# Kernel tuning notes

Measured on AMD Instinct MI355X. Metric: run time of the kernel, lower is better.

## Reference

```python
import jax, jax.numpy as jnp
import numpy as np

B, T, C, H = 2, 2048, 1024, 16
D = C // H
THETA = 10000.0


def setup_inputs() -> dict:
    key = jax.random.key(0)
    k1, k2, k3 = jax.random.split(key, 3)
    x = jax.random.normal(k1, (B, T, C), dtype=jnp.float32)
    tok_mask = jnp.ones((B, T), dtype=bool)
    # torch Linear weights stored transposed: y = x @ W.T; we store [in, out]
    W_qkv = jax.random.normal(k2, (C, 3 * C), dtype=jnp.float32) / np.sqrt(C)
    W_o = jax.random.normal(k3, (C, C), dtype=jnp.float32) / np.sqrt(C)
    return {"x": x, "tok_mask": tok_mask, "W_qkv": W_qkv, "W_o": W_o}


def _rope_tables(t_len):
    # NOTE: source uses exponents arange(1, D+1, 2)/D and positions starting at 1
    exps = jnp.arange(1, D + 1, 2, dtype=jnp.float32)[: D // 2] / D
    w = 1.0 / (THETA ** exps)                      # [D/2]
    t = jnp.arange(1, t_len + 1, dtype=jnp.float32)  # [T]
    ang = t[:, None] * w[None, :]                  # [T, D/2]
    return jnp.sin(ang), jnp.cos(ang)


def _rope(x, sin, cos):
    # x: [B, H, T, D]; rotate interleaved pairs
    x1 = x[..., ::2]
    x2 = x[..., 1::2]
    r1 = x1 * cos - x2 * sin
    r2 = x1 * sin + x2 * cos
    return jnp.stack((r1, r2), axis=-1).reshape(x.shape)


def reference(x, tok_mask, W_qkv, W_o):
    b, t, c = x.shape
    qkv = x @ W_qkv                                   # [B,T,3C]
    q, k, v = jnp.split(qkv, 3, axis=-1)
    def heads(z):
        return z.reshape(b, t, H, D).transpose(0, 2, 1, 3)  # [B,H,T,D]
    q, k, v = heads(q), heads(k), heads(v)
    sin, cos = _rope_tables(t)
    q = _rope(q, sin, cos)
    k = _rope(k, sin, cos)
    scores = jnp.einsum('bhqd,bhkd->bhqk', q, k) / jnp.sqrt(jnp.float32(D))
    # mask[b,i,j] = tok_mask[b,i] & tok_mask[b,j] & causal
    mask = tok_mask[:, None, :, None] & tok_mask[:, None, None, :]  # [B,1,T,T]
    causal = jnp.tril(jnp.ones((t, t), dtype=bool))
    mask = mask & causal[None, None, :, :]
    scores = jnp.where(mask, scores, jnp.float32(-1e9))
    att = jax.nn.softmax(scores, axis=-1)             # dropout p=0 (eval)
    y = jnp.einsum('bhqk,bhkd->bhqd', att, v)
    y = y.transpose(0, 2, 1, 3).reshape(b, t, c)
    return y @ W_o
```

## Files before the change

kernel.cpp:

```cpp
#include <hip/hip_runtime.h>
#include <hip/hip_bf16.h>

typedef __bf16 bf16x8 __attribute__((ext_vector_type(8)));
typedef short s16x4 __attribute__((ext_vector_type(4)));
typedef float floatx4 __attribute__((ext_vector_type(4)));
typedef __hip_bfloat16 bf16;

#define T_SEQ 2048
#define NH 16
#define HD 64
#define CDIM 1024

__device__ __forceinline__ void gload16(const bf16* g, bf16* ldsbase) {
  __builtin_amdgcn_global_load_lds((const __attribute__((address_space(1))) void*)g,
                                   (__attribute__((address_space(3))) void*)ldsbase, 16, 0, 0);
}

__global__ __launch_bounds__(256) void prep_kernel(const float* __restrict__ x,
                                                   const float* __restrict__ Wqkv,
                                                   const float* __restrict__ Wo,
                                                   bf16* __restrict__ Xb,
                                                   bf16* __restrict__ WqkvT,
                                                   bf16* __restrict__ WoT,
                                                   float2* __restrict__ tab) {
  __shared__ float tile[32][33];
  const int bid = blockIdx.x, tid = threadIdx.x;
  if (bid < 4096) {
    int i = bid * 256 + tid;
    const float4 v = ((const float4*)x)[i];
    union { bf16 h[4]; uint2 u; } pk;
    pk.h[0] = __float2bfloat16(v.x);
    pk.h[1] = __float2bfloat16(v.y);
    pk.h[2] = __float2bfloat16(v.z);
    pk.h[3] = __float2bfloat16(v.w);
    ((uint2*)Xb)[i] = pk.u;
  } else if (bid < 8192) {
    const float* in;
    bf16* out;
    int bx, by, R, Cc;
    if (bid < 7168) {
      int t = bid - 4096;
      in = Wqkv; out = WqkvT; R = 1024; Cc = 3072;
      bx = (t % 96) * 32; by = (t / 96) * 32;
    } else {
      int t = bid - 7168;
      in = Wo; out = WoT; R = 1024; Cc = 1024;
      bx = (t & 31) * 32; by = (t >> 5) * 32;
    }
    const int tx = tid & 31, ty = tid >> 5;
#pragma unroll
    for (int i = 0; i < 32; i += 8)
      tile[ty + i][tx] = in[(size_t)(by + ty + i) * Cc + bx + tx];
    __syncthreads();
#pragma unroll
    for (int i = 0; i < 32; i += 8)
      out[(size_t)(bx + ty + i) * R + by + tx] = __float2bfloat16(tile[tx][ty + i]);
  } else {
    int idx = (bid - 8192) * 256 + tid;
    int t = idx >> 5, j = idx & 31;
    float w = exp2f(-13.287712379549449f * (float)(2 * j + 1) * (1.0f / 64.0f));
    float ang = (float)(t + 1) * w;
    tab[idx] = make_float2(cosf(ang), sinf(ang));
  }
}

template <int MODE>
__global__ __launch_bounds__(256) void gemm_bt(
    const bf16* __restrict__ A, const bf16* __restrict__ BT, float* __restrict__ CoutF,
    const float2* __restrict__ tab, bf16* __restrict__ Qr, bf16* __restrict__ Kr,
    bf16* __restrict__ Vt, int M, int N, int K) {
  constexpr int LDK = 64;
  __shared__ __align__(16) bf16 As[128 * LDK];
  __shared__ __align__(16) bf16 Bs[128 * LDK];
  const int tid = threadIdx.x, lane = tid & 63, wave = tid >> 6;
  const int quad = lane >> 4, c16 = lane & 15;
  const int tile_m = blockIdx.y * 128, tile_n = blockIdx.x * 128;
  const int wm = (wave >> 1) * 64, wn = (wave & 1) * 64;
  const int r0 = tid >> 3;
  const int csw = ((tid & 7) ^ (r0 & 7)) * 8;
  const int s1 = (quad ^ (c16 & 7)) * 8;
  const int s2 = s1 ^ 32;
  floatx4 acc[4][4] = {};
  for (int k0 = 0; k0 < K; k0 += 64) {
    __syncthreads();
#pragma unroll
    for (int i = 0; i < 4; i++) {
      gload16(&A[(size_t)(tile_m + r0 + i * 32) * K + k0 + csw], &As[i * 2048 + wave * 512]);
      gload16(&BT[(size_t)(tile_n + r0 + i * 32) * K + k0 + csw], &Bs[i * 2048 + wave * 512]);
    }
    __syncthreads();
    bf16x8 af[4], bfr[4];
#pragma unroll
    for (int i = 0; i < 4; i++) {
      af[i] = *(const bf16x8*)&As[(wm + i * 16 + c16) * LDK + s1];
      bfr[i] = *(const bf16x8*)&Bs[(wn + i * 16 + c16) * LDK + s1];
    }
#pragma unroll
    for (int mi = 0; mi < 4; mi++)
#pragma unroll
      for (int ni = 0; ni < 4; ni++)
        acc[mi][ni] = __builtin_amdgcn_mfma_f32_16x16x32_bf16(af[mi], bfr[ni], acc[mi][ni], 0, 0, 0);
#pragma unroll
    for (int i = 0; i < 4; i++) {
      af[i] = *(const bf16x8*)&As[(wm + i * 16 + c16) * LDK + s2];
      bfr[i] = *(const bf16x8*)&Bs[(wn + i * 16 + c16) * LDK + s2];
    }
#pragma unroll
    for (int mi = 0; mi < 4; mi++)
#pragma unroll
      for (int ni = 0; ni < 4; ni++)
        acc[mi][ni] = __builtin_amdgcn_mfma_f32_16x16x32_bf16(af[mi], bfr[ni], acc[mi][ni], 0, 0, 0);
  }
  if (MODE == 0) {
#pragma unroll
    for (int mi = 0; mi < 4; mi++) {
      int row0 = tile_m + wm + mi * 16 + quad * 4;
#pragma unroll
      for (int ni = 0; ni < 4; ni++) {
        int col = tile_n + wn + ni * 16 + c16;
#pragma unroll
        for (int r = 0; r < 4; r++)
          CoutF[(size_t)(row0 + r) * N + col] = acc[mi][ni][r];
      }
    }
  } else {
#pragma unroll
    for (int ni = 0; ni < 4; ni++) {
      int colg = tile_n + wn + ni * 16 + c16;
      int seg = colg >> 10;
      int cc = colg & 1023;
      int h = cc >> 6, d = cc & 63, j = d >> 1;
#pragma unroll
      for (int mi = 0; mi < 4; mi++) {
        int row0 = tile_m + wm + mi * 16 + quad * 4;
#pragma unroll
        for (int r = 0; r < 4; r++) {
          int rowg = row0 + r;
          int b = rowg >> 11, t = rowg & 2047;
          float val = acc[mi][ni][r];
          float partner = __shfl_xor(val, 1, 64);
          size_t bh = (size_t)(b * NH + h);
          if (seg == 2) {
            Vt[(bh * HD + d) * T_SEQ + t] = __float2bfloat16(val);
          } else {
            float2 sc = tab[t * 32 + j];
            float outv = ((d & 1) == 0) ? (val * sc.x - partner * sc.y)
                                        : (val * sc.x + partner * sc.y);
            if (seg == 0) outv *= 0.125f;
            bf16* dst = (seg == 0) ? Qr : Kr;
            dst[(bh * T_SEQ + t) * HD + d] = __float2bfloat16(outv);
          }
        }
      }
    }
  }
}

__global__ __launch_bounds__(256) void attn_kernel(const bf16* __restrict__ Qr,
                                                   const bf16* __restrict__ Kr,
                                                   const bf16* __restrict__ Vt,
                                                   bf16* __restrict__ Y) {
  constexpr int DPAD = 68;
  constexpr float FM = 5.0f;
  __shared__ __align__(16) bf16 Ks0[64 * DPAD], Ks1[64 * DPAD];
  __shared__ __align__(16) bf16 Vs0[64 * DPAD], Vs1[64 * DPAD];
  __shared__ __align__(16) bf16 Ps0[4][16 * DPAD], Ps1[4][16 * DPAD];
  const int qtile = 31 - (blockIdx.x >> 5), bh = blockIdx.x & 31;
  const int b = bh >> 4, h = bh & 15;
  const int tid = threadIdx.x, lane = tid & 63, wave = tid >> 6;
  const int quad = lane >> 4, c16 = lane & 15;
  const size_t hoff = (size_t)bh * T_SEQ * HD;
  const int row0 = tid >> 3, cp = tid & 7;
  const int qbase = qtile * 64;
  const int qg = qbase + wave * 16 + c16;
  bf16x8 qf0 = *(const bf16x8*)&Qr[hoff + (size_t)qg * HD + quad * 8];
  bf16x8 qf1 = *(const bf16x8*)&Qr[hoff + (size_t)qg * HD + 32 + quad * 8];
  floatx4 o_acc[4] = {};
  float l_run = 0.f;
  const int n_st = (qtile + 2) >> 1;
  bf16x8 kreg0 = *(const bf16x8*)&Kr[hoff + (size_t)row0 * HD + cp * 8];
  bf16x8 kreg1 = *(const bf16x8*)&Kr[hoff + (size_t)(row0 + 32) * HD + cp * 8];
  bf16x8 kreg2 = *(const bf16x8*)&Kr[hoff + (size_t)(row0 + 64) * HD + cp * 8];
  bf16x8 kreg3 = *(const bf16x8*)&Kr[hoff + (size_t)(row0 + 96) * HD + cp * 8];
  bf16x8 vreg0 = *(const bf16x8*)&Vt[hoff + (size_t)row0 * T_SEQ + cp * 8];
  bf16x8 vreg1 = *(const bf16x8*)&Vt[hoff + (size_t)(row0 + 32) * T_SEQ + cp * 8];
  bf16x8 vreg2 = *(const bf16x8*)&Vt[hoff + (size_t)row0 * T_SEQ + 64 + cp * 8];
  bf16x8 vreg3 = *(const bf16x8*)&Vt[hoff + (size_t)(row0 + 32) * T_SEQ + 64 + cp * 8];
  for (int st = 0; st < n_st; ++st) {
    const int sbase = st * 128;
    *(bf16x8*)&Ks0[row0 * DPAD + cp * 8] = kreg0;
    *(bf16x8*)&Ks0[(row0 + 32) * DPAD + cp * 8] = kreg1;
    *(bf16x8*)&Ks1[row0 * DPAD + cp * 8] = kreg2;
    *(bf16x8*)&Ks1[(row0 + 32) * DPAD + cp * 8] = kreg3;
    *(bf16x8*)&Vs0[row0 * DPAD + cp * 8] = vreg0;
    *(bf16x8*)&Vs0[(row0 + 32) * DPAD + cp * 8] = vreg1;
    *(bf16x8*)&Vs1[row0 * DPAD + cp * 8] = vreg2;
    *(bf16x8*)&Vs1[(row0 + 32) * DPAD + cp * 8] = vreg3;
    __syncthreads();
    if (st + 1 < n_st) {
      const int nb = sbase + 128;
      kreg0 = *(const bf16x8*)&Kr[hoff + (size_t)(nb + row0) * HD + cp * 8];
      kreg1 = *(const bf16x8*)&Kr[hoff + (size_t)(nb + row0 + 32) * HD + cp * 8];
      kreg2 = *(const bf16x8*)&Kr[hoff + (size_t)(nb + row0 + 64) * HD + cp * 8];
      kreg3 = *(const bf16x8*)&Kr[hoff + (size_t)(nb + row0 + 96) * HD + cp * 8];
      vreg0 = *(const bf16x8*)&Vt[hoff + (size_t)row0 * T_SEQ + nb + cp * 8];
      vreg1 = *(const bf16x8*)&Vt[hoff + (size_t)(row0 + 32) * T_SEQ + nb + cp * 8];
      vreg2 = *(const bf16x8*)&Vt[hoff + (size_t)row0 * T_SEQ + nb + 64 + cp * 8];
      vreg3 = *(const bf16x8*)&Vt[hoff + (size_t)(row0 + 32) * T_SEQ + nb + 64 + cp * 8];
    }
    floatx4 s[8];
#pragma unroll
    for (int nt = 0; nt < 4; nt++) {
      bf16x8 kf0 = *(const bf16x8*)&Ks0[(nt * 16 + c16) * DPAD + quad * 8];
      bf16x8 kf1 = *(const bf16x8*)&Ks0[(nt * 16 + c16) * DPAD + 32 + quad * 8];
      floatx4 z = {0.f, 0.f, 0.f, 0.f};
      z = __builtin_amdgcn_mfma_f32_16x16x32_bf16(kf0, qf0, z, 0, 0, 0);
      z = __builtin_amdgcn_mfma_f32_16x16x32_bf16(kf1, qf1, z, 0, 0, 0);
      s[nt] = z;
    }
#pragma unroll
    for (int nt = 0; nt < 4; nt++) {
      bf16x8 kf0 = *(const bf16x8*)&Ks1[(nt * 16 + c16) * DPAD + quad * 8];
      bf16x8 kf1 = *(const bf16x8*)&Ks1[(nt * 16 + c16) * DPAD + 32 + quad * 8];
      floatx4 z = {0.f, 0.f, 0.f, 0.f};
      z = __builtin_amdgcn_mfma_f32_16x16x32_bf16(kf0, qf0, z, 0, 0, 0);
      z = __builtin_amdgcn_mfma_f32_16x16x32_bf16(kf1, qf1, z, 0, 0, 0);
      s[4 + nt] = z;
    }
    const bool maskt = (st == n_st - 1);
#pragma unroll
    for (int i = 0; i < 8; i++) {
      union { bf16 h[4]; s16x4 sv; } ph;
#pragma unroll
      for (int r = 0; r < 4; r++) {
        float pp = __expf(s[i][r] - FM);
        if (maskt) {
          int kg = sbase + i * 16 + quad * 4 + r;
          pp = (kg <= qg) ? pp : 0.f;
        }
        l_run += pp;
        ph.h[r] = __float2bfloat16(pp);
      }
      if (i < 4)
        *(s16x4*)&Ps0[wave][c16 * DPAD + i * 16 + quad * 4] = ph.sv;
      else
        *(s16x4*)&Ps1[wave][c16 * DPAD + (i - 4) * 16 + quad * 4] = ph.sv;
    }
    bf16x8 pf00 = *(const bf16x8*)&Ps0[wave][c16 * DPAD + quad * 8];
    bf16x8 pf01 = *(const bf16x8*)&Ps0[wave][c16 * DPAD + 32 + quad * 8];
    bf16x8 pf10 = *(const bf16x8*)&Ps1[wave][c16 * DPAD + quad * 8];
    bf16x8 pf11 = *(const bf16x8*)&Ps1[wave][c16 * DPAD + 32 + quad * 8];
#pragma unroll
    for (int dt = 0; dt < 4; dt++) {
      bf16x8 vf0 = *(const bf16x8*)&Vs0[(dt * 16 + c16) * DPAD + quad * 8];
      bf16x8 vf1 = *(const bf16x8*)&Vs0[(dt * 16 + c16) * DPAD + 32 + quad * 8];
      bf16x8 vf2 = *(const bf16x8*)&Vs1[(dt * 16 + c16) * DPAD + quad * 8];
      bf16x8 vf3 = *(const bf16x8*)&Vs1[(dt * 16 + c16) * DPAD + 32 + quad * 8];
      o_acc[dt] = __builtin_amdgcn_mfma_f32_16x16x32_bf16(pf00, vf0, o_acc[dt], 0, 0, 0);
      o_acc[dt] = __builtin_amdgcn_mfma_f32_16x16x32_bf16(pf01, vf1, o_acc[dt], 0, 0, 0);
      o_acc[dt] = __builtin_amdgcn_mfma_f32_16x16x32_bf16(pf10, vf2, o_acc[dt], 0, 0, 0);
      o_acc[dt] = __builtin_amdgcn_mfma_f32_16x16x32_bf16(pf11, vf3, o_acc[dt], 0, 0, 0);
    }
    __syncthreads();
  }
  l_run += __shfl_xor(l_run, 16, 64);
  l_run += __shfl_xor(l_run, 32, 64);
  float linv = 1.0f / l_run;
  float l_bc[4];
#pragma unroll
  for (int r = 0; r < 4; r++) l_bc[r] = __shfl(linv, quad * 4 + r, 16);
#pragma unroll
  for (int dt = 0; dt < 4; dt++)
#pragma unroll
    for (int r = 0; r < 4; r++) {
      int t = qbase + wave * 16 + quad * 4 + r;
      Y[((size_t)(b * T_SEQ + t)) * CDIM + h * HD + dt * 16 + c16] =
          __float2bfloat16(o_acc[dt][r] * l_bc[r]);
    }
}

extern "C" void kernel_launch(void* const* d_in, const int* in_sizes, int n_in,
                              void* d_out, int out_size, void* d_ws, size_t ws_size,
                              hipStream_t stream) {
  const float* x    = (const float*)d_in[0];
  const float* Wqkv = (const float*)d_in[2];
  const float* Wo   = (const float*)d_in[3];
  float* out = (float*)d_out;

  bf16* ws    = (bf16*)d_ws;
  bf16* Xb    = ws;
  bf16* WqkvT = Xb + 4194304;
  bf16* WoT   = WqkvT + 3072 * 1024;
  bf16* Qr    = WoT + 1024 * 1024;
  bf16* Kr    = Qr + 4194304;
  bf16* Vt    = Kr + 4194304;
  bf16* Y     = Vt + 4194304;
  float2* tab = (float2*)(Y + 4194304);

  prep_kernel<<<dim3(8448), 256, 0, stream>>>(x, Wqkv, Wo, Xb, WqkvT, WoT, tab);
  gemm_bt<1><<<dim3(3072 / 128, 4096 / 128), 256, 0, stream>>>(
      Xb, WqkvT, nullptr, tab, Qr, Kr, Vt, 4096, 3072, 1024);
  attn_kernel<<<dim3(1024), 256, 0, stream>>>(Qr, Kr, Vt, Y);
  gemm_bt<0><<<dim3(1024 / 128, 4096 / 128), 256, 0, stream>>>(
      Y, WoT, out, nullptr, nullptr, nullptr, nullptr, 4096, 1024, 1024);
}
```

Measured before the change: 193.8 us.

## Stage GEMM epilogues through LDS for coalesced vector stores, store Q transposed

Both GEMM epilogues now write accumulators into shared memory and then issue 16-byte coalesced global stores. Previously each lane scattered individual scalar stores, including strided transposed writes for V. Q is now stored transposed ([bh, d, t]) like V, and the attention kernel gathers its Q fragments with scalar strided loads. The extra LDS round trips and barriers, and the uncoalesced Q gathers in attention, are traded for far fewer scattered global writes.

```diff
diff --git a/kernel.cpp b/kernel.cpp
--- a/kernel.cpp
+++ b/kernel.cpp
@@ -67,11 +67,13 @@
 template <int MODE>
 __global__ __launch_bounds__(256) void gemm_bt(
     const bf16* __restrict__ A, const bf16* __restrict__ BT, float* __restrict__ CoutF,
-    const float2* __restrict__ tab, bf16* __restrict__ Qr, bf16* __restrict__ Kr,
+    const float2* __restrict__ tab, bf16* __restrict__ Qt, bf16* __restrict__ Kr,
     bf16* __restrict__ Vt, int M, int N, int K) {
   constexpr int LDK = 64;
-  __shared__ __align__(16) bf16 As[128 * LDK];
-  __shared__ __align__(16) bf16 Bs[128 * LDK];
+  constexpr int PADC = 136;
+  __shared__ __align__(16) bf16 smem[17408];
+  bf16* As = smem;
+  bf16* Bs = smem + 128 * LDK;
   const int tid = threadIdx.x, lane = tid & 63, wave = tid >> 6;
   const int quad = lane >> 4, c16 = lane & 15;
   const int tile_m = blockIdx.y * 128, tile_n = blockIdx.x * 128;
@@ -111,52 +113,110 @@
       for (int ni = 0; ni < 4; ni++)
         acc[mi][ni] = __builtin_amdgcn_mfma_f32_16x16x32_bf16(af[mi], bfr[ni], acc[mi][ni], 0, 0, 0);
   }
+  __syncthreads();
   if (MODE == 0) {
-#pragma unroll
-    for (int mi = 0; mi < 4; mi++) {
-      int row0 = tile_m + wm + mi * 16 + quad * 4;
-#pragma unroll
-      for (int ni = 0; ni < 4; ni++) {
-        int col = tile_n + wn + ni * 16 + c16;
-#pragma unroll
-        for (int r = 0; r < 4; r++)
-          CoutF[(size_t)(row0 + r) * N + col] = acc[mi][ni][r];
-      }
-    }
-  } else {
-#pragma unroll
-    for (int ni = 0; ni < 4; ni++) {
-      int colg = tile_n + wn + ni * 16 + c16;
-      int seg = colg >> 10;
-      int cc = colg & 1023;
-      int h = cc >> 6, d = cc & 63, j = d >> 1;
-#pragma unroll
-      for (int mi = 0; mi < 4; mi++) {
-        int row0 = tile_m + wm + mi * 16 + quad * 4;
-#pragma unroll
-        for (int r = 0; r < 4; r++) {
-          int rowg = row0 + r;
-          int b = rowg >> 11, t = rowg & 2047;
-          float val = acc[mi][ni][r];
-          float partner = __shfl_xor(val, 1, 64);
-          size_t bh = (size_t)(b * NH + h);
-          if (seg == 2) {
-            Vt[(bh * HD + d) * T_SEQ + t] = __float2bfloat16(val);
-          } else {
-            float2 sc = tab[t * 32 + j];
-            float outv = ((d & 1) == 0) ? (val * sc.x - partner * sc.y)
-                                        : (val * sc.x + partner * sc.y);
-            if (seg == 0) outv *= 0.125f;
-            bf16* dst = (seg == 0) ? Qr : Kr;
-            dst[(bh * T_SEQ + t) * HD + d] = __float2bfloat16(outv);
+    float* Ctf = (float*)smem;
+#pragma unroll
+    for (int p = 0; p < 2; p++) {
+      if ((wave >> 1) == p) {
+#pragma unroll
+        for (int mi = 0; mi < 4; mi++) {
+          int rl = mi * 16 + quad * 4;
+#pragma unroll
+          for (int ni = 0; ni < 4; ni++) {
+            int col = wn + ni * 16 + c16;
+#pragma unroll
+            for (int r = 0; r < 4; r++)
+              Ctf[(rl + r) * 132 + col] = acc[mi][ni][r];
           }
         }
       }
-    }
-  }
-}
-
-__global__ __launch_bounds__(256) void attn_kernel(const bf16* __restrict__ Qr,
+      __syncthreads();
+#pragma unroll
+      for (int i = 0; i < 8; i++) {
+        int e = tid + i * 256;
+        int row = e >> 5, cb = (e & 31) * 4;
+        floatx4 v4 = *(const floatx4*)&Ctf[row * 132 + cb];
+        *(floatx4*)&CoutF[(size_t)(tile_m + p * 64 + row) * N + tile_n + cb] = v4;
+      }
+      __syncthreads();
+    }
+  } else {
+    const int seg = tile_n >> 10;
+    const int bq = tile_m >> 11;
+    const int tg0 = tile_m & 2047;
+    bf16* Ct = smem;
+    if (seg != 1) {
+#pragma unroll
+      for (int ni = 0; ni < 4; ni++) {
+        const int col = wn + ni * 16 + c16;
+        const int cc = (tile_n + col) & 1023;
+        const int j = (cc & 63) >> 1;
+#pragma unroll
+        for (int mi = 0; mi < 4; mi++) {
+          const int row0 = wm + mi * 16 + quad * 4;
+          union { bf16 h[4]; s16x4 sv; } ph;
+#pragma unroll
+          for (int r = 0; r < 4; r++) {
+            float val = acc[mi][ni][r];
+            float outv;
+            if (seg == 0) {
+              float partner = __shfl_xor(val, 1, 64);
+              float2 sc = tab[(tg0 + row0 + r) * 32 + j];
+              outv = (((cc & 1) == 0) ? (val * sc.x - partner * sc.y)
+                                      : (val * sc.x + partner * sc.y)) * 0.125f;
+            } else {
+              outv = val;
+            }
+            ph.h[r] = __float2bfloat16(outv);
+          }
+          *(s16x4*)&Ct[col * PADC + row0] = ph.sv;
+        }
+      }
+      __syncthreads();
+      bf16* dst = (seg == 0) ? Qt : Vt;
+#pragma unroll
+      for (int i = 0; i < 8; i++) {
+        int e = tid + i * 256;
+        int col = e >> 4, tb = (e & 15) * 8;
+        bf16x8 vv = *(const bf16x8*)&Ct[col * PADC + tb];
+        int h = ((tile_n & 1023) + col) >> 6, d = col & 63;
+        *(bf16x8*)&dst[((size_t)(bq * NH + h) * HD + d) * T_SEQ + tg0 + tb] = vv;
+      }
+    } else {
+#pragma unroll
+      for (int ni = 0; ni < 4; ni++) {
+        const int col = wn + ni * 16 + c16;
+        const int cc = (tile_n + col) & 1023;
+        const int j = (cc & 63) >> 1;
+#pragma unroll
+        for (int mi = 0; mi < 4; mi++) {
+          const int row0 = wm + mi * 16 + quad * 4;
+#pragma unroll
+          for (int r = 0; r < 4; r++) {
+            float val = acc[mi][ni][r];
+            float partner = __shfl_xor(val, 1, 64);
+            float2 sc = tab[(tg0 + row0 + r) * 32 + j];
+            float outv = ((cc & 1) == 0) ? (val * sc.x - partner * sc.y)
+                                         : (val * sc.x + partner * sc.y);
+            Ct[(row0 + r) * PADC + col] = __float2bfloat16(outv);
+          }
+        }
+      }
+      __syncthreads();
+#pragma unroll
+      for (int i = 0; i < 8; i++) {
+        int e = tid + i * 256;
+        int row = e >> 4, db = (e & 15) * 8;
+        bf16x8 vv = *(const bf16x8*)&Ct[row * PADC + db];
+        int h = ((tile_n & 1023) + db) >> 6, d = db & 63;
+        *(bf16x8*)&Kr[((size_t)(bq * NH + h) * T_SEQ + tg0 + row) * HD + d] = vv;
+      }
+    }
+  }
+}
+
+__global__ __launch_bounds__(256) void attn_kernel(const bf16* __restrict__ Qt,
                                                    const bf16* __restrict__ Kr,
                                                    const bf16* __restrict__ Vt,
                                                    bf16* __restrict__ Y) {
@@ -173,8 +233,12 @@
   const int row0 = tid >> 3, cp = tid & 7;
   const int qbase = qtile * 64;
   const int qg = qbase + wave * 16 + c16;
-  bf16x8 qf0 = *(const bf16x8*)&Qr[hoff + (size_t)qg * HD + quad * 8];
-  bf16x8 qf1 = *(const bf16x8*)&Qr[hoff + (size_t)qg * HD + 32 + quad * 8];
+  bf16x8 qf0, qf1;
+#pragma unroll
+  for (int j = 0; j < 8; j++) {
+    qf0[j] = *(const __bf16*)&Qt[hoff + (size_t)(quad * 8 + j) * T_SEQ + qg];
+    qf1[j] = *(const __bf16*)&Qt[hoff + (size_t)(quad * 8 + 32 + j) * T_SEQ + qg];
+  }
   floatx4 o_acc[4] = {};
   float l_run = 0.f;
   const int n_st = (qtile + 2) >> 1;
@@ -291,16 +355,16 @@
   bf16* Xb    = ws;
   bf16* WqkvT = Xb + 4194304;
   bf16* WoT   = WqkvT + 3072 * 1024;
-  bf16* Qr    = WoT + 1024 * 1024;
-  bf16* Kr    = Qr + 4194304;
+  bf16* Qt    = WoT + 1024 * 1024;
+  bf16* Kr    = Qt + 4194304;
   bf16* Vt    = Kr + 4194304;
   bf16* Y     = Vt + 4194304;
   float2* tab = (float2*)(Y + 4194304);
 
   prep_kernel<<<dim3(8448), 256, 0, stream>>>(x, Wqkv, Wo, Xb, WqkvT, WoT, tab);
   gemm_bt<1><<<dim3(3072 / 128, 4096 / 128), 256, 0, stream>>>(
-      Xb, WqkvT, nullptr, tab, Qr, Kr, Vt, 4096, 3072, 1024);
-  attn_kernel<<<dim3(1024), 256, 0, stream>>>(Qr, Kr, Vt, Y);
+      Xb, WqkvT, nullptr, tab, Qt, Kr, Vt, 4096, 3072, 1024);
+  attn_kernel<<<dim3(1024), 256, 0, stream>>>(Qt, Kr, Vt, Y);
   gemm_bt<0><<<dim3(1024 / 128, 4096 / 128), 256, 0, stream>>>(
       Y, WoT, out, nullptr, nullptr, nullptr, nullptr, 4096, 1024, 1024);
 }
```

Measured after the change: 193.2 us. About the same (-0.3%).
